# Kernel optimization log

Hardware: AMD Instinct MI355X
Metric: run time of the kernel (lower is better)

Reference implementation:

```python
import jax, jax.numpy as jnp
import numpy as np

DIM = 2048
N_HEADS = 16
HEAD_DIM = DIM // N_HEADS
B, S = 2, 2048


def apply_rotary(x, cos, sin):
    # x: [..., dim]; cos/sin broadcast to [..., dim//2]
    # even/odd interleaved rotation, matching the torch ::2 / 1::2 indexing
    xe = x[..., 0::2]
    xo = x[..., 1::2]
    oe = xe * cos - xo * sin
    oo = xo * cos + xe * sin
    return jnp.stack([oe, oo], axis=-1).reshape(x.shape)


def setup_inputs() -> dict:
    key = jax.random.key(0)
    ks = jax.random.split(key, 12)
    scale = 1.0 / np.sqrt(DIM)
    x = jax.random.normal(ks[0], (B, S, DIM), dtype=jnp.float32)
    cos = jax.random.normal(ks[1], (S, DIM // 2), dtype=jnp.float32)
    sin = jax.random.normal(ks[2], (S, DIM // 2), dtype=jnp.float32)
    mask = jnp.zeros((1, 1, S, S), dtype=jnp.float32)
    Wq = jax.random.normal(ks[3], (DIM, DIM), dtype=jnp.float32) * scale
    bq = jnp.zeros((DIM,), dtype=jnp.float32)
    Wk = jax.random.normal(ks[4], (DIM, DIM), dtype=jnp.float32) * scale
    bk = jnp.zeros((DIM,), dtype=jnp.float32)
    Wv = jax.random.normal(ks[5], (DIM, DIM), dtype=jnp.float32) * scale
    bv = jnp.zeros((DIM,), dtype=jnp.float32)
    Wo = jax.random.normal(ks[6], (DIM, DIM), dtype=jnp.float32) * scale
    bo = jnp.zeros((DIM,), dtype=jnp.float32)
    return {"x": x, "cos": cos, "sin": sin, "mask": mask,
            "Wq": Wq, "bq": bq, "Wk": Wk, "bk": bk,
            "Wv": Wv, "bv": bv, "Wo": Wo, "bo": bo}


def reference(x, cos, sin, mask, Wq, bq, Wk, bk, Wv, bv, Wo, bo):
    # Linear projections (torch nn.Linear: y = x @ W.T + b)
    q = jnp.einsum('bsd,ed->bse', x, Wq) + bq
    k = jnp.einsum('bsd,ed->bse', x, Wk) + bk
    v = jnp.einsum('bsd,ed->bse', x, Wv) + bv
    # RoPE on full dim, then split into heads (faithful to source ordering)
    q = apply_rotary(q, cos, sin).reshape(B, S, N_HEADS, HEAD_DIM)
    k = apply_rotary(k, cos, sin).reshape(B, S, N_HEADS, HEAD_DIM)
    v = v.reshape(B, S, N_HEADS, HEAD_DIM)
    scale = 1.0 / jnp.sqrt(jnp.float32(HEAD_DIM))
    attn = jnp.einsum('bqhd,bkhd->bhqk', q, k) * scale  # [B,H,S,S]
    attn = attn + mask
    attn = jax.nn.softmax(attn, axis=-1)
    out = jnp.einsum('bhqk,bkhd->bqhd', attn, v).reshape(B, S, DIM)
    return jnp.einsum('bsd,ed->bse', out, Wo) + bo
```

## Files before the change

### kernel.cpp

```cpp
#include <hip/hip_runtime.h>

#define DIM   2048
#define SLEN  2048
#define BATCH 2
#define NHEAD 16
#define HDIM  128
#define MROWS (BATCH*SLEN)

typedef __attribute__((ext_vector_type(8))) __bf16 bf16x8;
typedef __attribute__((ext_vector_type(4))) float  f32x4;
typedef __attribute__((ext_vector_type(8))) unsigned short u16x8;
typedef __attribute__((ext_vector_type(4))) unsigned short u16x4;

__device__ __forceinline__ unsigned short f2bf(float f) {
  union { float f; unsigned u; } v; v.f = f;
  unsigned r = v.u + 0x7FFFu + ((v.u >> 16) & 1u);
  return (unsigned short)(r >> 16);
}
__device__ __forceinline__ float bf2f(unsigned short h) {
  union { unsigned u; float f; } v; v.u = ((unsigned)h) << 16;
  return v.f;
}
__device__ __forceinline__ void gload16(const void* g, void* l) {
  __builtin_amdgcn_global_load_lds(
      (const __attribute__((address_space(1))) void*)g,
      (__attribute__((address_space(3))) void*)l, 16, 0, 0);
}

__global__ __launch_bounds__(256) void conv_f32_bf16(
    const float* __restrict__ in, unsigned short* __restrict__ out, int n4) {
  int t = blockIdx.x * 256 + threadIdx.x;
  if (t >= n4) return;
  f32x4 v = *(const f32x4*)(in + (size_t)t * 4);
  u16x4 o;
  o[0] = f2bf(v[0]); o[1] = f2bf(v[1]); o[2] = f2bf(v[2]); o[3] = f2bf(v[3]);
  *(u16x4*)(out + (size_t)t * 4) = o;
}

template<int OUT_MODE>
__global__ __launch_bounds__(256) void gemm_bt(
    const unsigned short* __restrict__ A,
    const unsigned short* __restrict__ Bw,
    const float* __restrict__ bias,
    void* __restrict__ Cout, int M, int N, int K)
{
  __shared__ __align__(16) unsigned short As[128][32];
  __shared__ __align__(16) unsigned short Bs[128][32];
  const int tid  = threadIdx.x;
  const int lane = tid & 63;
  const int wid  = tid >> 6;
  const int wr   = wid >> 1, wc = wid & 1;
  const int lrow = lane >> 4, lcol = lane & 15;

  const int gx = gridDim.x;
  int bid = blockIdx.y * gx + blockIdx.x;
  int nwg = gx * gridDim.y;
  int swz = (bid & 7) * (nwg >> 3) + (bid >> 3);
  const int row0 = (swz % gx) * 128, col0 = (swz / gx) * 128;

  f32x4 acc[4][4] = {};

  const unsigned short* Ablk = A  + (size_t)row0 * K;
  const unsigned short* Bblk = Bw + (size_t)col0 * K;
  char* AsB = (char*)&As[0][0];
  char* BsB = (char*)&Bs[0][0];

  for (int k0 = 0; k0 < K; k0 += 32) {
#pragma unroll
    for (int r = 0; r < 2; ++r) {
      int f = r * 256 + tid;
      gload16(Ablk + (size_t)(f >> 2) * K + k0 + (f & 3) * 8, AsB + (r * 256 + wid * 64) * 16);
      gload16(Bblk + (size_t)(f >> 2) * K + k0 + (f & 3) * 8, BsB + (r * 256 + wid * 64) * 16);
    }
    __syncthreads();
    bf16x8 af[4], bfv[4];
#pragma unroll
    for (int m = 0; m < 4; ++m)
      af[m] = *(const bf16x8*)&As[wr * 64 + m * 16 + lcol][lrow * 8];
#pragma unroll
    for (int n = 0; n < 4; ++n)
      bfv[n] = *(const bf16x8*)&Bs[wc * 64 + n * 16 + lcol][lrow * 8];
#pragma unroll
    for (int m = 0; m < 4; ++m)
#pragma unroll
      for (int n = 0; n < 4; ++n)
        acc[m][n] = __builtin_amdgcn_mfma_f32_16x16x32_bf16(af[m], bfv[n], acc[m][n], 0, 0, 0);
    __syncthreads();
  }

#pragma unroll
  for (int m = 0; m < 4; ++m) {
#pragma unroll
    for (int n = 0; n < 4; ++n) {
      int col = col0 + wc * 64 + n * 16 + lcol;
      float bv = bias[col];
      if (OUT_MODE == 2) {
        int row = row0 + wr * 64 + m * 16 + lrow * 4;
        u16x4 o;
#pragma unroll
        for (int j = 0; j < 4; ++j) o[j] = f2bf(acc[m][n][j] + bv);
        *(u16x4*)((unsigned short*)Cout +
                  ((size_t)((row >> 11) * DIM + col)) * SLEN + (row & (SLEN - 1))) = o;
      } else {
#pragma unroll
        for (int j = 0; j < 4; ++j) {
          int row = row0 + wr * 64 + m * 16 + lrow * 4 + j;
          float val = acc[m][n][j] + bv;
          if (OUT_MODE == 1) ((unsigned short*)Cout)[(size_t)row * N + col] = f2bf(val);
          else               ((float*)Cout)[(size_t)row * N + col] = val;
        }
      }
    }
  }
}

__global__ __launch_bounds__(256) void gemm_qkv(
    const unsigned short* __restrict__ A,
    const unsigned short* __restrict__ Bw3,
    const float* __restrict__ bq, const float* __restrict__ bk, const float* __restrict__ bv,
    const float* __restrict__ cosT, const float* __restrict__ sinT, float qscale,
    unsigned short* __restrict__ qout,
    unsigned short* __restrict__ kout,
    unsigned short* __restrict__ vtout)
{
  __shared__ __align__(16) unsigned short As[128][32];
  __shared__ __align__(16) unsigned short Bs[128][32];
  const int tid  = threadIdx.x;
  const int lane = tid & 63;
  const int wid  = tid >> 6;
  const int wr   = wid >> 1, wc = wid & 1;
  const int lrow = lane >> 4, lcol = lane & 15;

  int bid = blockIdx.y * 32 + blockIdx.x;
  int swz = (bid & 7) * 192 + (bid >> 3);
  const int row0 = (swz & 31) * 128;
  const int by   = swz >> 5;
  const int seg  = by >> 4;
  const int col0 = (by & 15) * 128;

  f32x4 acc[4][4] = {};

  const unsigned short* Ablk = A   + (size_t)row0 * DIM;
  const unsigned short* Bblk = Bw3 + (size_t)by * 128 * DIM;
  char* AsB = (char*)&As[0][0];
  char* BsB = (char*)&Bs[0][0];

  for (int k0 = 0; k0 < DIM; k0 += 32) {
#pragma unroll
    for (int r = 0; r < 2; ++r) {
      int f = r * 256 + tid;
      gload16(Ablk + (size_t)(f >> 2) * DIM + k0 + (f & 3) * 8, AsB + (r * 256 + wid * 64) * 16);
      gload16(Bblk + (size_t)(f >> 2) * DIM + k0 + (f & 3) * 8, BsB + (r * 256 + wid * 64) * 16);
    }
    __syncthreads();
    bf16x8 af[4], bfv[4];
#pragma unroll
    for (int m = 0; m < 4; ++m)
      af[m] = *(const bf16x8*)&As[wr * 64 + m * 16 + lcol][lrow * 8];
#pragma unroll
    for (int n = 0; n < 4; ++n)
      bfv[n] = *(const bf16x8*)&Bs[wc * 64 + n * 16 + lcol][lrow * 8];
#pragma unroll
    for (int m = 0; m < 4; ++m)
#pragma unroll
      for (int n = 0; n < 4; ++n)
        acc[m][n] = __builtin_amdgcn_mfma_f32_16x16x32_bf16(af[m], bfv[n], acc[m][n], 0, 0, 0);
    __syncthreads();
  }

  if (seg == 2) {
#pragma unroll
    for (int m = 0; m < 4; ++m) {
#pragma unroll
      for (int n = 0; n < 4; ++n) {
        int col = col0 + wc * 64 + n * 16 + lcol;
        float bvv = bv[col];
        int row = row0 + wr * 64 + m * 16 + lrow * 4;
        u16x4 o;
#pragma unroll
        for (int j = 0; j < 4; ++j) o[j] = f2bf(acc[m][n][j] + bvv);
        *(u16x4*)(vtout + ((size_t)((row >> 11) * DIM + col)) * SLEN + (row & (SLEN - 1))) = o;
      }
    }
  } else {
    unsigned short* out = (seg == 0) ? qout : kout;
    const float* bias   = (seg == 0) ? bq : bk;
    const float  osc    = (seg == 0) ? qscale : 1.0f;
#pragma unroll
    for (int m = 0; m < 4; ++m) {
#pragma unroll
      for (int n = 0; n < 4; ++n) {
        int col = col0 + wc * 64 + n * 16 + lcol;
        float bvv = bias[col];
        int ip  = col >> 1;
        int odd = col & 1;
#pragma unroll
        for (int j = 0; j < 4; ++j) {
          int row = row0 + wr * 64 + m * 16 + lrow * 4 + j;
          int s   = row & (SLEN - 1);
          float v = acc[m][n][j] + bvv;
          float p = __shfl_xor(v, 1, 64);
          float c  = cosT[(size_t)s * (DIM / 2) + ip];
          float sn = sinT[(size_t)s * (DIM / 2) + ip];
          float o  = odd ? (v * c + p * sn) : (v * c - p * sn);
          out[(size_t)row * DIM + col] = f2bf(o * osc);
        }
      }
    }
  }
}

__global__ __launch_bounds__(256) void rope_inplace(
    unsigned short* __restrict__ q,
    const float* __restrict__ cosT, const float* __restrict__ sinT, float scale) {
  int t   = blockIdx.x * 256 + threadIdx.x;
  int row = t >> 8;
  int e0  = (t & 255) * 8;
  int s   = row & (SLEN - 1);
  unsigned short* p = q + (size_t)row * DIM + e0;
  u16x8 v = *(u16x8*)p;
  f32x4 c  = *(const f32x4*)(cosT + (size_t)s * (DIM / 2) + (e0 >> 1));
  f32x4 sn = *(const f32x4*)(sinT + (size_t)s * (DIM / 2) + (e0 >> 1));
#pragma unroll
  for (int i = 0; i < 4; ++i) {
    float xe = bf2f(v[2 * i]), xo = bf2f(v[2 * i + 1]);
    float oe = (xe * c[i] - xo * sn[i]) * scale;
    float oo = (xo * c[i] + xe * sn[i]) * scale;
    v[2 * i] = f2bf(oe); v[2 * i + 1] = f2bf(oo);
  }
  *(u16x8*)p = v;
}

__global__ __launch_bounds__(256) void attn_fwd(
    const unsigned short* __restrict__ Q,
    const unsigned short* __restrict__ Kg,
    const unsigned short* __restrict__ VtG,
    const float* __restrict__ mask,
    unsigned short* __restrict__ O)
{
  __shared__ __align__(16) unsigned short Ks[64][128];
  __shared__ __align__(16) unsigned short Vts[128][64];
  __shared__ __align__(16) unsigned short Ps[4][16][64];

  int s0 = blockIdx.x + 32 * (blockIdx.y + 16 * blockIdx.z);
  int xc = s0 & 7, jj = s0 >> 3;
  int pane = xc * 4 + (jj >> 5);
  const int qt = jj & 31;
  const int h  = pane & 15, b = pane >> 4;

  const int tid = threadIdx.x, lane = tid & 63, wid = tid >> 6;
  const int lrow = lane >> 4, lcol = lane & 15;
  const int sx = (lcol & 7) << 4;

  const unsigned short* Qb  = Q  + ((size_t)(b * SLEN + qt * 64)) * DIM + h * HDIM;
  const unsigned short* Kb  = Kg + (size_t)(b * SLEN) * DIM + h * HDIM;
  const unsigned short* Vtb = VtG + ((size_t)(b * DIM + h * HDIM)) * SLEN;
  const float* maskRow = mask + (size_t)(qt * 64 + wid * 16 + lcol) * SLEN;

  bf16x8 qf[4];
#pragma unroll
  for (int kk = 0; kk < 4; ++kk)
    qf[kk] = *(const bf16x8*)(Qb + (size_t)(wid * 16 + lcol) * DIM + kk * 32 + lrow * 8);

  float m_run = -1e30f, l_run = 0.f;
  f32x4 acc_o[8] = {};

  char* KsB  = (char*)&Ks[0][0];
  char* VtsB = (char*)&Vts[0][0];
  char* PsB  = (char*)&Ps[0][0][0];

  for (int kt = 0; kt < SLEN / 64; ++kt) {
    __syncthreads();
#pragma unroll
    for (int r = 0; r < 4; ++r) {
      int L = r * 256 + wid * 64 + lane;
      int krow = L >> 4, kc = (L & 15) ^ (krow & 7);
      gload16(Kb + (size_t)(kt * 64 + krow) * DIM + kc * 8,
              KsB + (size_t)(r * 256 + wid * 64) * 16);
    }
#pragma unroll
    for (int r = 0; r < 4; ++r) {
      int L = r * 256 + wid * 64 + lane;
      int d = L >> 3, vc = (L & 7) ^ (d & 7);
      gload16(Vtb + (size_t)d * SLEN + kt * 64 + vc * 8,
              VtsB + (size_t)(r * 256 + wid * 64) * 16);
    }
    __syncthreads();

    f32x4 sacc[4] = {};
#pragma unroll
    for (int kn = 0; kn < 4; ++kn)
#pragma unroll
      for (int kk = 0; kk < 4; ++kk) {
        bf16x8 kf = *(const bf16x8*)(KsB + (size_t)(kn * 16 + lcol) * 256
                                         + ((kk * 64 + lrow * 16) ^ sx));
        sacc[kn] = __builtin_amdgcn_mfma_f32_16x16x32_bf16(kf, qf[kk], sacc[kn], 0, 0, 0);
      }

    float sv[16];
#pragma unroll
    for (int kn = 0; kn < 4; ++kn) {
      f32x4 mv = *(const f32x4*)(maskRow + kt * 64 + kn * 16 + lrow * 4);
#pragma unroll
      for (int r = 0; r < 4; ++r) sv[kn * 4 + r] = sacc[kn][r] + mv[r];
    }

    float pmax = sv[0];
#pragma unroll
    for (int i = 1; i < 16; ++i) pmax = fmaxf(pmax, sv[i]);
    pmax = fmaxf(pmax, __shfl_xor(pmax, 16, 64));
    pmax = fmaxf(pmax, __shfl_xor(pmax, 32, 64));

    if (!__all(pmax - m_run <= 8.0f)) {
      float mnew = fmaxf(m_run, pmax);
      float alpha = __expf(m_run - mnew);
      m_run = mnew;
      l_run *= alpha;
      float ar[4];
#pragma unroll
      for (int r = 0; r < 4; ++r) ar[r] = __shfl(alpha, lrow * 4 + r, 64);
#pragma unroll
      for (int d = 0; d < 8; ++d) {
        f32x4 t = acc_o[d];
#pragma unroll
        for (int r = 0; r < 4; ++r) t[r] *= ar[r];
        acc_o[d] = t;
      }
    }

    float pv[16];
    float rsum = 0.f;
#pragma unroll
    for (int i = 0; i < 16; ++i) { float pe = __expf(sv[i] - m_run); pv[i] = pe; rsum += pe; }
    rsum += __shfl_xor(rsum, 16, 64);
    rsum += __shfl_xor(rsum, 32, 64);
    l_run += rsum;

#pragma unroll
    for (int kn = 0; kn < 4; ++kn)
#pragma unroll
      for (int r = 0; r < 4; ++r)
        *(unsigned short*)(PsB + wid * 2048 + lcol * 128
                           + ((kn * 32 + (lrow * 4 + r) * 2) ^ sx)) = f2bf(pv[kn * 4 + r]);

    bf16x8 pf[2];
#pragma unroll
    for (int ks = 0; ks < 2; ++ks)
      pf[ks] = *(const bf16x8*)(PsB + wid * 2048 + lcol * 128
                                + ((ks * 64 + lrow * 16) ^ sx));
#pragma unroll
    for (int d = 0; d < 8; ++d)
#pragma unroll
      for (int ks = 0; ks < 2; ++ks) {
        bf16x8 vf = *(const bf16x8*)(VtsB + (size_t)(d * 16 + lcol) * 128
                                          + ((ks * 64 + lrow * 16) ^ sx));
        acc_o[d] = __builtin_amdgcn_mfma_f32_16x16x32_bf16(pf[ks], vf, acc_o[d], 0, 0, 0);
      }
  }

  float linv[4];
#pragma unroll
  for (int r = 0; r < 4; ++r) linv[r] = 1.0f / __shfl(l_run, lrow * 4 + r, 64);
  int orow0 = b * SLEN + qt * 64 + wid * 16 + lrow * 4;
#pragma unroll
  for (int d = 0; d < 8; ++d)
#pragma unroll
    for (int r = 0; r < 4; ++r) {
      float o = acc_o[d][r] * linv[r];
      O[(size_t)(orow0 + r) * DIM + h * HDIM + d * 16 + lcol] = f2bf(o);
    }
}

extern "C" void kernel_launch(void* const* d_in, const int* in_sizes, int n_in,
                              void* d_out, int out_size, void* d_ws, size_t ws_size,
                              hipStream_t stream) {
  const float* x    = (const float*)d_in[0];
  const float* cosT = (const float*)d_in[1];
  const float* sinT = (const float*)d_in[2];
  const float* mask = (const float*)d_in[3];
  const float* Wq   = (const float*)d_in[4];
  const float* bq   = (const float*)d_in[5];
  const float* Wk   = (const float*)d_in[6];
  const float* bk   = (const float*)d_in[7];
  const float* Wv   = (const float*)d_in[8];
  const float* bv   = (const float*)d_in[9];
  const float* Wo   = (const float*)d_in[10];
  const float* bo   = (const float*)d_in[11];

  const size_t MB = 1u << 20;
  if (ws_size < 72 * MB) return;

  char* ws = (char*)d_ws;
  unsigned short* xb = (unsigned short*)(ws);
  unsigned short* qb = (unsigned short*)(ws + 16 * MB);
  unsigned short* kb = (unsigned short*)(ws + 32 * MB);
  unsigned short* Vt = (unsigned short*)(ws + 48 * MB);
  unsigned short* Ob = xb;

  const float scale = 0.08838834764831845f;
  conv_f32_bf16<<<8192, 256, 0, stream>>>(x, xb, (MROWS * DIM) / 4);

  if (ws_size >= 88 * MB) {
    unsigned short* Wb3 = (unsigned short*)(ws + 64 * MB);
    conv_f32_bf16<<<4096, 256, 0, stream>>>(Wq, Wb3, (DIM * DIM) / 4);
    conv_f32_bf16<<<4096, 256, 0, stream>>>(Wk, Wb3 + (size_t)DIM * DIM, (DIM * DIM) / 4);
    conv_f32_bf16<<<4096, 256, 0, stream>>>(Wv, Wb3 + (size_t)2 * DIM * DIM, (DIM * DIM) / 4);
    gemm_qkv<<<dim3(MROWS / 128, 48), 256, 0, stream>>>(xb, Wb3, bq, bk, bv,
                                                        cosT, sinT, scale, qb, kb, Vt);
    attn_fwd<<<dim3(SLEN / 64, NHEAD, BATCH), 256, 0, stream>>>(qb, kb, Vt, mask, Ob);
    conv_f32_bf16<<<4096, 256, 0, stream>>>(Wo, Wb3, (DIM * DIM) / 4);
    gemm_bt<0><<<dim3(MROWS / 128, DIM / 128), 256, 0, stream>>>(Ob, Wb3, bo, d_out, MROWS, DIM, DIM);
  } else {
    unsigned short* Wb = (unsigned short*)(ws + 64 * MB);
    dim3 gGemm(MROWS / 128, DIM / 128);
    conv_f32_bf16<<<4096, 256, 0, stream>>>(Wq, Wb, (DIM * DIM) / 4);
    gemm_bt<1><<<gGemm, 256, 0, stream>>>(xb, Wb, bq, qb, MROWS, DIM, DIM);
    conv_f32_bf16<<<4096, 256, 0, stream>>>(Wk, Wb, (DIM * DIM) / 4);
    gemm_bt<1><<<gGemm, 256, 0, stream>>>(xb, Wb, bk, kb, MROWS, DIM, DIM);
    conv_f32_bf16<<<4096, 256, 0, stream>>>(Wv, Wb, (DIM * DIM) / 4);
    gemm_bt<2><<<gGemm, 256, 0, stream>>>(xb, Wb, bv, Vt, MROWS, DIM, DIM);
    rope_inplace<<<4096, 256, 0, stream>>>(qb, cosT, sinT, scale);
    rope_inplace<<<4096, 256, 0, stream>>>(kb, cosT, sinT, 1.0f);
    attn_fwd<<<dim3(SLEN / 64, NHEAD, BATCH), 256, 0, stream>>>(qb, kb, Vt, mask, Ob);
    conv_f32_bf16<<<4096, 256, 0, stream>>>(Wo, Wb, (DIM * DIM) / 4);
    gemm_bt<0><<<gGemm, 256, 0, stream>>>(Ob, Wb, bo, d_out, MROWS, DIM, DIM);
  }
}
```

Before: 404.2 us.

## Give each attention wave two 16-row query slabs, halving block size to 128 threads

The attention kernel now runs 2 waves per block instead of 4, with each wave handling 32 query rows as two 16-row sub-tiles. Each K fragment read from shared memory feeds two MFMAs, and each V fragment likewise, halving LDS reads per unit of MFMA work. P is now written to shared memory with 4-wide vector stores. In exchange, per-wave register use roughly doubles (two accumulator sets and softmax states), which may lower occupancy, and fewer waves share each K/V tile load.

```diff
diff --git a/kernel.cpp b/kernel.cpp
--- a/kernel.cpp
+++ b/kernel.cpp
@@ -231,7 +231,7 @@
   *(u16x8*)p = v;
 }
 
-__global__ __launch_bounds__(256) void attn_fwd(
+__global__ __launch_bounds__(128) void attn_fwd(
     const unsigned short* __restrict__ Q,
     const unsigned short* __restrict__ Kg,
     const unsigned short* __restrict__ VtG,
@@ -240,7 +240,7 @@
 {
   __shared__ __align__(16) unsigned short Ks[64][128];
   __shared__ __align__(16) unsigned short Vts[128][64];
-  __shared__ __align__(16) unsigned short Ps[4][16][64];
+  __shared__ __align__(16) unsigned short Ps[2][32][64];
 
   int s0 = blockIdx.x + 32 * (blockIdx.y + 16 * blockIdx.z);
   int xc = s0 & 7, jj = s0 >> 3;
@@ -252,18 +252,20 @@
   const int lrow = lane >> 4, lcol = lane & 15;
   const int sx = (lcol & 7) << 4;
 
-  const unsigned short* Qb  = Q  + ((size_t)(b * SLEN + qt * 64)) * DIM + h * HDIM;
+  const unsigned short* Qb  = Q  + ((size_t)(b * SLEN + qt * 64 + wid * 32)) * DIM + h * HDIM;
   const unsigned short* Kb  = Kg + (size_t)(b * SLEN) * DIM + h * HDIM;
   const unsigned short* Vtb = VtG + ((size_t)(b * DIM + h * HDIM)) * SLEN;
-  const float* maskRow = mask + (size_t)(qt * 64 + wid * 16 + lcol) * SLEN;
-
-  bf16x8 qf[4];
-#pragma unroll
-  for (int kk = 0; kk < 4; ++kk)
-    qf[kk] = *(const bf16x8*)(Qb + (size_t)(wid * 16 + lcol) * DIM + kk * 32 + lrow * 8);
-
-  float m_run = -1e30f, l_run = 0.f;
-  f32x4 acc_o[8] = {};
+  const float* mrow0 = mask + (size_t)(qt * 64 + wid * 32 + lcol) * SLEN;
+
+  bf16x8 qf[2][4];
+#pragma unroll
+  for (int qs = 0; qs < 2; ++qs)
+#pragma unroll
+    for (int kk = 0; kk < 4; ++kk)
+      qf[qs][kk] = *(const bf16x8*)(Qb + (size_t)(qs * 16 + lcol) * DIM + kk * 32 + lrow * 8);
+
+  float m_run[2] = {-1e30f, -1e30f}, l_run[2] = {0.f, 0.f};
+  f32x4 acc_o[2][8] = {};
 
   char* KsB  = (char*)&Ks[0][0];
   char* VtsB = (char*)&Vts[0][0];
@@ -272,103 +274,114 @@
   for (int kt = 0; kt < SLEN / 64; ++kt) {
     __syncthreads();
 #pragma unroll
-    for (int r = 0; r < 4; ++r) {
-      int L = r * 256 + wid * 64 + lane;
+    for (int r = 0; r < 8; ++r) {
+      int L = r * 128 + tid;
       int krow = L >> 4, kc = (L & 15) ^ (krow & 7);
       gload16(Kb + (size_t)(kt * 64 + krow) * DIM + kc * 8,
-              KsB + (size_t)(r * 256 + wid * 64) * 16);
-    }
-#pragma unroll
-    for (int r = 0; r < 4; ++r) {
-      int L = r * 256 + wid * 64 + lane;
+              KsB + (size_t)(r * 128 + wid * 64) * 16);
+    }
+#pragma unroll
+    for (int r = 0; r < 8; ++r) {
+      int L = r * 128 + tid;
       int d = L >> 3, vc = (L & 7) ^ (d & 7);
       gload16(Vtb + (size_t)d * SLEN + kt * 64 + vc * 8,
-              VtsB + (size_t)(r * 256 + wid * 64) * 16);
-    }
-    __syncthreads();
-
-    f32x4 sacc[4] = {};
+              VtsB + (size_t)(r * 128 + wid * 64) * 16);
+    }
+    __syncthreads();
+
+    f32x4 sacc[2][4] = {};
 #pragma unroll
     for (int kn = 0; kn < 4; ++kn)
 #pragma unroll
       for (int kk = 0; kk < 4; ++kk) {
         bf16x8 kf = *(const bf16x8*)(KsB + (size_t)(kn * 16 + lcol) * 256
                                          + ((kk * 64 + lrow * 16) ^ sx));
-        sacc[kn] = __builtin_amdgcn_mfma_f32_16x16x32_bf16(kf, qf[kk], sacc[kn], 0, 0, 0);
-      }
-
-    float sv[16];
-#pragma unroll
-    for (int kn = 0; kn < 4; ++kn) {
-      f32x4 mv = *(const f32x4*)(maskRow + kt * 64 + kn * 16 + lrow * 4);
-#pragma unroll
-      for (int r = 0; r < 4; ++r) sv[kn * 4 + r] = sacc[kn][r] + mv[r];
-    }
-
-    float pmax = sv[0];
-#pragma unroll
-    for (int i = 1; i < 16; ++i) pmax = fmaxf(pmax, sv[i]);
-    pmax = fmaxf(pmax, __shfl_xor(pmax, 16, 64));
-    pmax = fmaxf(pmax, __shfl_xor(pmax, 32, 64));
-
-    if (!__all(pmax - m_run <= 8.0f)) {
-      float mnew = fmaxf(m_run, pmax);
-      float alpha = __expf(m_run - mnew);
-      m_run = mnew;
-      l_run *= alpha;
-      float ar[4];
-#pragma unroll
-      for (int r = 0; r < 4; ++r) ar[r] = __shfl(alpha, lrow * 4 + r, 64);
-#pragma unroll
-      for (int d = 0; d < 8; ++d) {
-        f32x4 t = acc_o[d];
-#pragma unroll
-        for (int r = 0; r < 4; ++r) t[r] *= ar[r];
-        acc_o[d] = t;
-      }
-    }
-
-    float pv[16];
-    float rsum = 0.f;
-#pragma unroll
-    for (int i = 0; i < 16; ++i) { float pe = __expf(sv[i] - m_run); pv[i] = pe; rsum += pe; }
-    rsum += __shfl_xor(rsum, 16, 64);
-    rsum += __shfl_xor(rsum, 32, 64);
-    l_run += rsum;
-
-#pragma unroll
-    for (int kn = 0; kn < 4; ++kn)
-#pragma unroll
-      for (int r = 0; r < 4; ++r)
-        *(unsigned short*)(PsB + wid * 2048 + lcol * 128
-                           + ((kn * 32 + (lrow * 4 + r) * 2) ^ sx)) = f2bf(pv[kn * 4 + r]);
-
-    bf16x8 pf[2];
-#pragma unroll
-    for (int ks = 0; ks < 2; ++ks)
-      pf[ks] = *(const bf16x8*)(PsB + wid * 2048 + lcol * 128
-                                + ((ks * 64 + lrow * 16) ^ sx));
+        sacc[0][kn] = __builtin_amdgcn_mfma_f32_16x16x32_bf16(kf, qf[0][kk], sacc[0][kn], 0, 0, 0);
+        sacc[1][kn] = __builtin_amdgcn_mfma_f32_16x16x32_bf16(kf, qf[1][kk], sacc[1][kn], 0, 0, 0);
+      }
+
+#pragma unroll
+    for (int qs = 0; qs < 2; ++qs) {
+      float sv[16];
+#pragma unroll
+      for (int kn = 0; kn < 4; ++kn) {
+        f32x4 mv = *(const f32x4*)(mrow0 + (size_t)qs * 16 * SLEN + kt * 64 + kn * 16 + lrow * 4);
+#pragma unroll
+        for (int r = 0; r < 4; ++r) sv[kn * 4 + r] = sacc[qs][kn][r] + mv[r];
+      }
+
+      float pmax = sv[0];
+#pragma unroll
+      for (int i = 1; i < 16; ++i) pmax = fmaxf(pmax, sv[i]);
+      pmax = fmaxf(pmax, __shfl_xor(pmax, 16, 64));
+      pmax = fmaxf(pmax, __shfl_xor(pmax, 32, 64));
+
+      if (!__all(pmax - m_run[qs] <= 8.0f)) {
+        float mnew = fmaxf(m_run[qs], pmax);
+        float alpha = __expf(m_run[qs] - mnew);
+        m_run[qs] = mnew;
+        l_run[qs] *= alpha;
+        float ar[4];
+#pragma unroll
+        for (int r = 0; r < 4; ++r) ar[r] = __shfl(alpha, lrow * 4 + r, 64);
+#pragma unroll
+        for (int d = 0; d < 8; ++d) {
+          f32x4 t = acc_o[qs][d];
+#pragma unroll
+          for (int r = 0; r < 4; ++r) t[r] *= ar[r];
+          acc_o[qs][d] = t;
+        }
+      }
+
+      float rsum = 0.f;
+#pragma unroll
+      for (int i = 0; i < 16; ++i) { sv[i] = __expf(sv[i] - m_run[qs]); rsum += sv[i]; }
+      rsum += __shfl_xor(rsum, 16, 64);
+      rsum += __shfl_xor(rsum, 32, 64);
+      l_run[qs] += rsum;
+
+#pragma unroll
+      for (int kn = 0; kn < 4; ++kn) {
+        u16x4 o;
+#pragma unroll
+        for (int r = 0; r < 4; ++r) o[r] = f2bf(sv[kn * 4 + r]);
+        *(u16x4*)(PsB + wid * 4096 + (qs * 16 + lcol) * 128
+                  + ((kn * 32 + lrow * 8) ^ sx)) = o;
+      }
+    }
+
+    bf16x8 pf[2][2];
+#pragma unroll
+    for (int qs = 0; qs < 2; ++qs)
+#pragma unroll
+      for (int ks = 0; ks < 2; ++ks)
+        pf[qs][ks] = *(const bf16x8*)(PsB + wid * 4096 + (qs * 16 + lcol) * 128
+                                      + ((ks * 64 + lrow * 16) ^ sx));
 #pragma unroll
     for (int d = 0; d < 8; ++d)
 #pragma unroll
       for (int ks = 0; ks < 2; ++ks) {
         bf16x8 vf = *(const bf16x8*)(VtsB + (size_t)(d * 16 + lcol) * 128
                                           + ((ks * 64 + lrow * 16) ^ sx));
-        acc_o[d] = __builtin_amdgcn_mfma_f32_16x16x32_bf16(pf[ks], vf, acc_o[d], 0, 0, 0);
-      }
-  }
-
-  float linv[4];
-#pragma unroll
-  for (int r = 0; r < 4; ++r) linv[r] = 1.0f / __shfl(l_run, lrow * 4 + r, 64);
-  int orow0 = b * SLEN + qt * 64 + wid * 16 + lrow * 4;
-#pragma unroll
-  for (int d = 0; d < 8; ++d)
-#pragma unroll
-    for (int r = 0; r < 4; ++r) {
-      float o = acc_o[d][r] * linv[r];
-      O[(size_t)(orow0 + r) * DIM + h * HDIM + d * 16 + lcol] = f2bf(o);
-    }
+        acc_o[0][d] = __builtin_amdgcn_mfma_f32_16x16x32_bf16(pf[0][ks], vf, acc_o[0][d], 0, 0, 0);
+        acc_o[1][d] = __builtin_amdgcn_mfma_f32_16x16x32_bf16(pf[1][ks], vf, acc_o[1][d], 0, 0, 0);
+      }
+  }
+
+#pragma unroll
+  for (int qs = 0; qs < 2; ++qs) {
+    float linv[4];
+#pragma unroll
+    for (int r = 0; r < 4; ++r) linv[r] = 1.0f / __shfl(l_run[qs], lrow * 4 + r, 64);
+    int orow0 = b * SLEN + qt * 64 + wid * 32 + qs * 16 + lrow * 4;
+#pragma unroll
+    for (int d = 0; d < 8; ++d)
+#pragma unroll
+      for (int r = 0; r < 4; ++r) {
+        float o = acc_o[qs][d][r] * linv[r];
+        O[(size_t)(orow0 + r) * DIM + h * HDIM + d * 16 + lcol] = f2bf(o);
+      }
+  }
 }
 
 extern "C" void kernel_launch(void* const* d_in, const int* in_sizes, int n_in,
@@ -407,7 +420,7 @@
     conv_f32_bf16<<<4096, 256, 0, stream>>>(Wv, Wb3 + (size_t)2 * DIM * DIM, (DIM * DIM) / 4);
     gemm_qkv<<<dim3(MROWS / 128, 48), 256, 0, stream>>>(xb, Wb3, bq, bk, bv,
                                                         cosT, sinT, scale, qb, kb, Vt);
-    attn_fwd<<<dim3(SLEN / 64, NHEAD, BATCH), 256, 0, stream>>>(qb, kb, Vt, mask, Ob);
+    attn_fwd<<<dim3(SLEN / 64, NHEAD, BATCH), 128, 0, stream>>>(qb, kb, Vt, mask, Ob);
     conv_f32_bf16<<<4096, 256, 0, stream>>>(Wo, Wb3, (DIM * DIM) / 4);
     gemm_bt<0><<<dim3(MROWS / 128, DIM / 128), 256, 0, stream>>>(Ob, Wb3, bo, d_out, MROWS, DIM, DIM);
   } else {
@@ -421,7 +434,7 @@
     gemm_bt<2><<<gGemm, 256, 0, stream>>>(xb, Wb, bv, Vt, MROWS, DIM, DIM);
     rope_inplace<<<4096, 256, 0, stream>>>(qb, cosT, sinT, scale);
     rope_inplace<<<4096, 256, 0, stream>>>(kb, cosT, sinT, 1.0f);
-    attn_fwd<<<dim3(SLEN / 64, NHEAD, BATCH), 256, 0, stream>>>(qb, kb, Vt, mask, Ob);
+    attn_fwd<<<dim3(SLEN / 64, NHEAD, BATCH), 128, 0, stream>>>(qb, kb, Vt, mask, Ob);
     conv_f32_bf16<<<4096, 256, 0, stream>>>(Wo, Wb, (DIM * DIM) / 4);
     gemm_bt<0><<<gGemm, 256, 0, stream>>>(Ob, Wb, bo, d_out, MROWS, DIM, DIM);
   }
```

Measured after the change: 425.6 us. 1.05x slower.
